# Kernel tuning notes

Hardware: AMD Instinct MI355X
Metric: run time of the kernel (lower is better)

The kernel has to match this reference:

```python
import jax, jax.numpy as jnp
import numpy as np

D_MODEL = 1024
NUM_HEADS = 16
SEQ_LEN = 2048
WINDOW_SIZES = (5, 10, 20, 40)


def _avg_gaussian_mask(seq_len, dtype=jnp.float32):
    # mask[i,j] = exp(-(i-j)^2/(2 w^2)) if j <= i else 0; averaged over 4 windows.
    i = jnp.arange(seq_len, dtype=dtype)[:, None]
    j = jnp.arange(seq_len, dtype=dtype)[None, :]
    d2 = (i - j) ** 2
    lower = (j <= i)
    masks = [jnp.where(lower, jnp.exp(-d2 / (2.0 * w * w)), 0.0) for w in WINDOW_SIZES]
    return sum(masks) / len(WINDOW_SIZES)  # [S, S]


def setup_inputs() -> dict:
    key = jax.random.key(0)
    ks = jax.random.split(key, 11)
    B, S, D = 2, SEQ_LEN, D_MODEL
    std = 1.0 / np.sqrt(D)
    inp = {
        "Q": jax.random.normal(ks[0], (B, S, D), jnp.float32),
        "K": jax.random.normal(ks[1], (B, S, D), jnp.float32),
        "V": jax.random.normal(ks[2], (B, S, D), jnp.float32),
        "Wq": jax.random.uniform(ks[3], (D, D), jnp.float32, -std, std),
        "bq": jax.random.uniform(ks[4], (D,), jnp.float32, -std, std),
        "Wk": jax.random.uniform(ks[5], (D, D), jnp.float32, -std, std),
        "bk": jax.random.uniform(ks[6], (D,), jnp.float32, -std, std),
        "Wv": jax.random.uniform(ks[7], (D, D), jnp.float32, -std, std),
        "bv": jax.random.uniform(ks[8], (D,), jnp.float32, -std, std),
        "Wo": jax.random.uniform(ks[9], (D, D), jnp.float32, -std, std),
        "bo": jax.random.uniform(ks[10], (D,), jnp.float32, -std, std),
    }
    return inp


def reference(Q, K, V, Wq, bq, Wk, bk, Wv, bv, Wo, bo):
    B, S, D = Q.shape
    H, dk = NUM_HEADS, D // NUM_HEADS

    def proj(x, W, b):
        # torch Linear: x @ W^T + b, then split heads -> [B, H, S, dk]
        y = x @ W.T + b
        return y.reshape(B, S, H, dk).transpose(0, 2, 1, 3)

    q = proj(Q, Wq, bq)
    k = proj(K, Wk, bk)
    v = proj(V, Wv, bv)

    # mean over mask dim of (scores + mask_m) == scores + mean(mask)
    avg_mask = _avg_gaussian_mask(S, q.dtype)  # [S, S]
    scores = jnp.einsum('bhqd,bhkd->bhqk', q, k) / jnp.sqrt(jnp.asarray(dk, q.dtype))
    scores = scores + avg_mask  # broadcast over [B, H]
    probs = jax.nn.softmax(scores, axis=-1)
    out = jnp.einsum('bhqk,bhkd->bhqd', probs, v)
    out = out.transpose(0, 2, 1, 3).reshape(B, S, D)
    return out @ Wo.T + bo
```

## Files before the change

### kernel.cpp

```cpp
#include <hip/hip_runtime.h>
#include <hip/hip_bf16.h>


#define S_LEN 2048
#define D_MODEL 1024
#define NHEADS 16
#define DK 64
#define BATCH 2
#define M_ROWS (BATCH * S_LEN)
#define LOG2E 1.4426950408889634f

typedef float f32x4 __attribute__((ext_vector_type(4)));
typedef short s16x8 __attribute__((ext_vector_type(8)));
typedef unsigned short u16x4 __attribute__((ext_vector_type(4)));
typedef unsigned u32x2 __attribute__((ext_vector_type(2)));

__device__ __forceinline__ unsigned short f2bf(float f) {
    unsigned u = __builtin_bit_cast(unsigned, f);
    u = (u + 0x7FFFu + ((u >> 16) & 1u)) >> 16;
    return (unsigned short)u;
}

__device__ __forceinline__ float fast_exp2(float x) {
    float r;
    asm("v_exp_f32 %0, %1" : "=v"(r) : "v"(x));
    return r;
}

__device__ __forceinline__ unsigned cvt_pk_bf16(float a, float b) {
    unsigned r;
    asm("v_cvt_pk_bf16_f32 %0, %1, %2" : "=v"(r) : "v"(a), "v"(b));
    return r;
}

__device__ __forceinline__ float max3f(float a, float b, float c) {
    float r;
    asm("v_max3_f32 %0, %1, %2, %3" : "=v"(r) : "v"(a), "v"(b), "v"(c));
    return r;
}

#define GLD16(gptr, lptr)                                                     \
    __builtin_amdgcn_global_load_lds(                                         \
        (const __attribute__((address_space(1))) void*)(gptr),                \
        (__attribute__((address_space(3))) void*)(lptr), 16, 0, 0)

__global__ __launch_bounds__(256) void convert_kernel(
    const float* __restrict__ Q, const float* __restrict__ K,
    const float* __restrict__ V,
    const float* __restrict__ Wq, const float* __restrict__ Wk,
    const float* __restrict__ Wv, const float* __restrict__ Wo,
    unsigned short* __restrict__ Qb, unsigned short* __restrict__ Kb,
    unsigned short* __restrict__ Vb,
    unsigned short* __restrict__ Wqb, unsigned short* __restrict__ Wkb,
    unsigned short* __restrict__ Wvb, unsigned short* __restrict__ Wob,
    float* __restrict__ mtab)
{
    const int XN = M_ROWS * D_MODEL / 8;
    const int WN = D_MODEL * D_MODEL / 8;
    const int TOT = 3 * XN + 4 * WN;
    int i = blockIdx.x * 256 + threadIdx.x;
    if (i >= TOT) {
        int d = i - TOT;
        if (d < S_LEN) {
            float d2 = (float)d * (float)d;
            mtab[d] = LOG2E * 0.25f * (__expf(-d2 * (1.0f / 50.0f)) +
                                       __expf(-d2 * (1.0f / 200.0f)) +
                                       __expf(-d2 * (1.0f / 800.0f)) +
                                       __expf(-d2 * (1.0f / 3200.0f)));
        }
        return;
    }
    const float* src;
    unsigned short* dst;
    int off;
    if (i < 3 * XN) {
        if (i < XN)          { src = Q; dst = Qb; off = i; }
        else if (i < 2 * XN) { src = K; dst = Kb; off = i - XN; }
        else                 { src = V; dst = Vb; off = i - 2 * XN; }
    } else {
        int j = i - 3 * XN;
        if (j < WN)          { src = Wq; dst = Wqb; off = j; }
        else if (j < 2 * WN) { src = Wk; dst = Wkb; off = j - WN; }
        else if (j < 3 * WN) { src = Wv; dst = Wvb; off = j - 2 * WN; }
        else                 { src = Wo; dst = Wob; off = j - 3 * WN; }
    }
    f32x4 v0 = *(const f32x4*)(src + (size_t)off * 8);
    f32x4 v1 = *(const f32x4*)(src + (size_t)off * 8 + 4);
    s16x8 o;
#pragma unroll
    for (int j = 0; j < 4; ++j) {
        o[j]     = (short)f2bf(v0[j]);
        o[j + 4] = (short)f2bf(v1[j]);
    }
    *(s16x8*)(dst + (size_t)off * 8) = o;
}

__device__ __forceinline__ void gemm_core_128(
    const unsigned short* __restrict__ A, const unsigned short* __restrict__ B,
    unsigned short* As, unsigned short* Bs,
    int m0, int n0, int K, int tid, f32x4 acc[4][4])
{
    const int wid  = tid >> 6;
    const int lane = tid & 63;
    const int g    = lane >> 4;
    const int c    = lane & 15;
    const int wm   = wid >> 1;
    const int wn   = wid & 1;

    const int srow   = tid >> 3;
    const int schunk = tid & 7;

    for (int kt = 0; kt < K / 64; ++kt) {
        const int k0 = kt * 64;
        __syncthreads();
#pragma unroll
        for (int r = 0; r < 4; ++r) {
            const int row = r * 32 + srow;
            GLD16(A + (size_t)(m0 + row) * K + k0 + schunk * 8,
                  &As[(r * 256 + wid * 64) * 8]);
        }
#pragma unroll
        for (int r = 0; r < 4; ++r) {
            const int row = r * 32 + srow;
            GLD16(B + (size_t)(n0 + row) * K + k0 + schunk * 8,
                  &Bs[(r * 256 + wid * 64) * 8]);
        }
        __syncthreads();

        s16x8 a[2][4];
#pragma unroll
        for (int ks = 0; ks < 2; ++ks)
#pragma unroll
            for (int mf = 0; mf < 4; ++mf)
                a[ks][mf] = *(const s16x8*)
                    &As[(wm * 64 + mf * 16 + c) * 64 + ks * 32 + g * 8];
#pragma unroll
        for (int ks = 0; ks < 2; ++ks) {
#pragma unroll
            for (int nf = 0; nf < 4; ++nf) {
                s16x8 b = *(const s16x8*)
                    &Bs[(wn * 64 + nf * 16 + c) * 64 + ks * 32 + g * 8];
#pragma unroll
                for (int mf = 0; mf < 4; ++mf)
                    acc[mf][nf] = __builtin_amdgcn_mfma_f32_16x16x32_bf16(
                        a[ks][mf], b, acc[mf][nf], 0, 0, 0);
            }
        }
    }
}

__global__ __launch_bounds__(256) void proj_gemm(
    const unsigned short* __restrict__ Qx, const unsigned short* __restrict__ Kx,
    const unsigned short* __restrict__ Vx,
    const unsigned short* __restrict__ Wq, const unsigned short* __restrict__ Wk,
    const unsigned short* __restrict__ Wv,
    const float* __restrict__ bq, const float* __restrict__ bk,
    const float* __restrict__ bv,
    unsigned short* __restrict__ qo, unsigned short* __restrict__ ko,
    unsigned short* __restrict__ vo)
{
    const int z = blockIdx.z;
    const unsigned short* X = (z == 0) ? Qx : (z == 1) ? Kx : Vx;
    const unsigned short* W = (z == 0) ? Wq : (z == 1) ? Wk : Wv;
    const float* bias       = (z == 0) ? bq : (z == 1) ? bk : bv;
    unsigned short* out     = (z == 0) ? qo : (z == 1) ? ko : vo;
    const float scale = (z == 0) ? (0.125f * LOG2E) : 1.0f;

    __shared__ unsigned short As[128 * 64];
    __shared__ unsigned short Bs[128 * 64];

    const int tid = threadIdx.x;
    const int flat = blockIdx.y * 32 + blockIdx.x;
    const int sw   = (flat & 7) * 32 + (flat >> 3);
    const int m0   = (sw & 31) * 128;
    const int n0   = (sw >> 5) * 128;

    f32x4 acc[4][4];
#pragma unroll
    for (int i = 0; i < 4; ++i)
#pragma unroll
        for (int j = 0; j < 4; ++j) acc[i][j] = (f32x4){0.f, 0.f, 0.f, 0.f};

    gemm_core_128(X, W, As, Bs, m0, n0, D_MODEL, tid, acc);

    const int lane = tid & 63;
    const int g    = lane >> 4;
    const int c    = lane & 15;
    const int wm   = (tid >> 6) >> 1;
    const int wn   = (tid >> 6) & 1;

#pragma unroll
    for (int mf = 0; mf < 4; ++mf) {
#pragma unroll
        for (int nf = 0; nf < 4; ++nf) {
            const int o = n0 + wn * 64 + nf * 16 + c;
            const float bv_ = bias[o];
            const int h  = o >> 6;
            const int dd = o & 63;
#pragma unroll
            for (int r = 0; r < 4; ++r) {
                const int m = m0 + wm * 64 + mf * 16 + g * 4 + r;
                const int b = m >> 11;
                const int s = m & (S_LEN - 1);
                const float val = (acc[mf][nf][r] + bv_) * scale;
                out[(((size_t)(b * NHEADS + h)) * S_LEN + s) * DK + dd] = f2bf(val);
            }
        }
    }
}

__global__ __launch_bounds__(256) void out_gemm(
    const unsigned short* __restrict__ A,
    const unsigned short* __restrict__ W,
    const float* __restrict__ bias,
    float* __restrict__ out)
{
    __shared__ unsigned short As[128 * 64];
    __shared__ unsigned short Bs[128 * 64];

    const int tid = threadIdx.x;
    const int flat = blockIdx.y * 32 + blockIdx.x;
    const int sw   = (flat & 7) * 32 + (flat >> 3);
    const int m0   = (sw & 31) * 128;
    const int n0   = (sw >> 5) * 128;

    f32x4 acc[4][4];
#pragma unroll
    for (int i = 0; i < 4; ++i)
#pragma unroll
        for (int j = 0; j < 4; ++j) acc[i][j] = (f32x4){0.f, 0.f, 0.f, 0.f};

    gemm_core_128(A, W, As, Bs, m0, n0, D_MODEL, tid, acc);

    const int lane = tid & 63;
    const int g    = lane >> 4;
    const int c    = lane & 15;
    const int wm   = (tid >> 6) >> 1;
    const int wn   = (tid >> 6) & 1;

#pragma unroll
    for (int mf = 0; mf < 4; ++mf) {
#pragma unroll
        for (int nf = 0; nf < 4; ++nf) {
            const int o = n0 + wn * 64 + nf * 16 + c;
            const float bv_ = bias[o];
#pragma unroll
            for (int r = 0; r < 4; ++r) {
                const int m = m0 + wm * 64 + mf * 16 + g * 4 + r;
                out[(size_t)m * D_MODEL + o] = acc[mf][nf][r] + bv_;
            }
        }
    }
}

#define VSWZ(row) ((((row) >> 1) & 7) << 4)

__global__ __launch_bounds__(512) void attn_kernel(
    const unsigned short* __restrict__ qh,
    const unsigned short* __restrict__ kh,
    const unsigned short* __restrict__ vh,
    const float* __restrict__ mask_tab,
    unsigned short* __restrict__ attn_out)
{
    __shared__ float mtab[S_LEN];
    __shared__ unsigned short Kt[64 * 64];
    __shared__ unsigned short Vt[64 * 64];
    __shared__ unsigned short Pt[8][16 * 64];

    const int tid  = threadIdx.x;
    const int wid  = tid >> 6;
    const int lane = tid & 63;
    const int g    = lane >> 4;
    const int c    = lane & 15;

    const int flat = blockIdx.y * 16 + blockIdx.x;
    const int sw   = (flat & 7) * 64 + (flat >> 3);
    const int bh   = sw >> 4;
    const int bx   = sw & 15;
    const int b    = bh >> 4;
    const int h    = bh & 15;
    const int q0w  = bx * 128 + wid * 16;

    *(f32x4*)&mtab[tid * 4] = *(const f32x4*)&mask_tab[tid * 4];

    const size_t head_off = (size_t)bh * S_LEN * DK;
    const unsigned short* qp = qh + head_off;
    const unsigned short* kp = kh + head_off;
    const unsigned short* vp = vh + head_off;

    s16x8 aq[2];
    {
        const unsigned short* qrow = qp + (size_t)(q0w + c) * DK;
        aq[0] = *(const s16x8*)(qrow + g * 8);
        aq[1] = *(const s16x8*)(qrow + 32 + g * 8);
    }

    f32x4 acc_o[4];
#pragma unroll
    for (int nf = 0; nf < 4; ++nf) acc_o[nf] = (f32x4){0.f, 0.f, 0.f, 0.f};
    float m_l = -1e30f;
    f32x4 lsum = (f32x4){0.f, 0.f, 0.f, 0.f};

    const int srowK = tid >> 3;
    const int soffE = (tid & 7) * 8;
    const int vd0   = (tid & 31) * 2;
    const int vkq   = (tid >> 5) * 4;

    s16x8 kreg;
    unsigned vreg[4];
    kreg = *(const s16x8*)&kp[(size_t)srowK * DK + soffE];
#pragma unroll
    for (int i = 0; i < 4; ++i)
        vreg[i] = *(const unsigned*)&vp[(size_t)(vkq + i) * DK + vd0];

    unsigned short* Ptw = Pt[wid];

    for (int kt = 0; kt < S_LEN / 64; ++kt) {
        const int k0 = kt * 64;
        __syncthreads();

        *(s16x8*)((char*)Kt + srowK * 128 + ((soffE * 2) ^ ((srowK & 7) << 4))) = kreg;
        {
            u16x4 lo4, hi4;
#pragma unroll
            for (int i = 0; i < 4; ++i) {
                lo4[i] = (unsigned short)vreg[i];
                hi4[i] = (unsigned short)(vreg[i] >> 16);
            }
            *(u16x4*)((char*)Vt + vd0 * 128 + ((vkq * 2) ^ VSWZ(vd0))) = lo4;
            *(u16x4*)((char*)Vt + (vd0 + 1) * 128 +
                      ((vkq * 2) ^ VSWZ(vd0 + 1))) = hi4;
        }
        if (kt < S_LEN / 64 - 1) {
            const int k1 = k0 + 64;
            kreg = *(const s16x8*)&kp[(size_t)(k1 + srowK) * DK + soffE];
#pragma unroll
            for (int i = 0; i < 4; ++i)
                vreg[i] = *(const unsigned*)&vp[(size_t)(k1 + vkq + i) * DK + vd0];
        }
        __syncthreads();

        f32x4 st[4];
        __builtin_amdgcn_s_setprio(1);
#pragma unroll
        for (int nf = 0; nf < 4; ++nf) {
            st[nf] = (f32x4){0.f, 0.f, 0.f, 0.f};
#pragma unroll
            for (int f = 0; f < 2; ++f) {
                const int row = nf * 16 + c;
                s16x8 kf = *(const s16x8*)((const char*)Kt + row * 128 +
                                           ((f * 64 + g * 16) ^ ((row & 7) << 4)));
                st[nf] = __builtin_amdgcn_mfma_f32_16x16x32_bf16(
                    kf, aq[f], st[nf], 0, 0, 0);
            }
        }
        __builtin_amdgcn_s_setprio(0);

        const int diff = q0w - k0;
        if (diff >= -15 && diff <= 510) {
            const int dbase = q0w + c - k0;
#pragma unroll
            for (int nf = 0; nf < 4; ++nf) {
#pragma unroll
                for (int r = 0; r < 4; ++r) {
                    const int d = dbase - (nf * 16 + g * 4 + r);
                    if (d >= 0) st[nf][r] += mtab[d];
                }
            }
        }

        float tm = max3f(st[0][0], st[0][1], st[0][2]);
        tm = max3f(tm, st[0][3], st[1][0]);
        tm = max3f(tm, st[1][1], st[1][2]);
        tm = max3f(tm, st[1][3], st[2][0]);
        tm = max3f(tm, st[2][1], st[2][2]);
        tm = max3f(tm, st[2][3], st[3][0]);
        tm = max3f(tm, st[3][1], st[3][2]);
        tm = fmaxf(tm, st[3][3]);

        if (__any(tm > m_l + 8.0f)) {
            tm = fmaxf(tm, __shfl_xor(tm, 16));
            tm = fmaxf(tm, __shfl_xor(tm, 32));
            const float mnew = fmaxf(m_l, tm);
            const float csc  = fast_exp2(m_l - mnew);
            m_l = mnew;
            lsum *= csc;
            f32x4 cscv;
#pragma unroll
            for (int r = 0; r < 4; ++r) cscv[r] = __shfl(csc, g * 4 + r);
#pragma unroll
            for (int nf = 0; nf < 4; ++nf) acc_o[nf] *= cscv;
        }

#pragma unroll
        for (int nf = 0; nf < 4; ++nf)
#pragma unroll
            for (int r = 0; r < 4; ++r)
                st[nf][r] = fast_exp2(st[nf][r] - m_l);
        lsum += (st[0] + st[1]) + (st[2] + st[3]);

#pragma unroll
        for (int nf = 0; nf < 4; ++nf) {
            u32x2 pk;
            pk[0] = cvt_pk_bf16(st[nf][0], st[nf][1]);
            pk[1] = cvt_pk_bf16(st[nf][2], st[nf][3]);
            *(u32x2*)((char*)Ptw + c * 128 +
                      ((nf * 32 + g * 8) ^ ((c & 7) << 4))) = pk;
        }

        __builtin_amdgcn_s_setprio(1);
#pragma unroll
        for (int f = 0; f < 2; ++f) {
            s16x8 pa = *(const s16x8*)((const char*)Ptw + c * 128 +
                                       ((f * 64 + g * 16) ^ ((c & 7) << 4)));
#pragma unroll
            for (int nf = 0; nf < 4; ++nf) {
                const int row = nf * 16 + c;
                s16x8 vb = *(const s16x8*)((const char*)Vt + row * 128 +
                                           ((f * 64 + g * 16) ^ VSWZ(row)));
                acc_o[nf] = __builtin_amdgcn_mfma_f32_16x16x32_bf16(
                    pa, vb, acc_o[nf], 0, 0, 0);
            }
        }
        __builtin_amdgcn_s_setprio(0);
    }

    float l = (lsum[0] + lsum[1]) + (lsum[2] + lsum[3]);
    l += __shfl_xor(l, 16);
    l += __shfl_xor(l, 32);
    f32x4 linv;
#pragma unroll
    for (int r = 0; r < 4; ++r) linv[r] = 1.0f / __shfl(l, g * 4 + r);
#pragma unroll
    for (int nf = 0; nf < 4; ++nf) {
#pragma unroll
        for (int r = 0; r < 4; ++r) {
            const int i_glob = q0w + g * 4 + r;
            const int d = nf * 16 + c;
            attn_out[((size_t)(b * S_LEN + i_glob)) * D_MODEL + h * DK + d] =
                f2bf(acc_o[nf][r] * linv[r]);
        }
    }
}

extern "C" void kernel_launch(void* const* d_in, const int* in_sizes, int n_in,
                              void* d_out, int out_size, void* d_ws, size_t ws_size,
                              hipStream_t stream) {
    const float* Q  = (const float*)d_in[0];
    const float* K  = (const float*)d_in[1];
    const float* V  = (const float*)d_in[2];
    const float* Wq = (const float*)d_in[3];
    const float* bq = (const float*)d_in[4];
    const float* Wk = (const float*)d_in[5];
    const float* bk = (const float*)d_in[6];
    const float* Wv = (const float*)d_in[7];
    const float* bv = (const float*)d_in[8];
    const float* Wo = (const float*)d_in[9];
    const float* bo = (const float*)d_in[10];
    float* out = (float*)d_out;

    const size_t XE = (size_t)M_ROWS * D_MODEL;
    const size_t WE = (size_t)D_MODEL * D_MODEL;
    unsigned short* qh  = (unsigned short*)d_ws;
    unsigned short* kh  = qh + XE;
    unsigned short* vh  = kh + XE;
    unsigned short* ah  = vh + XE;
    unsigned short* Qb  = ah + XE;
    unsigned short* Kb  = Qb + XE;
    unsigned short* Vb  = Kb + XE;
    unsigned short* Wqb = Vb + XE;
    unsigned short* Wkb = Wqb + WE;
    unsigned short* Wvb = Wkb + WE;
    unsigned short* Wob = Wvb + WE;
    float* mtab = (float*)(Wob + WE);

    convert_kernel<<<dim3((3 * XE / 8 + 4 * WE / 8) / 256 + 8), 256, 0, stream>>>(
        Q, K, V, Wq, Wk, Wv, Wo, Qb, Kb, Vb, Wqb, Wkb, Wvb, Wob, mtab);
    proj_gemm<<<dim3(32, 8, 3), 256, 0, stream>>>(
        Qb, Kb, Vb, Wqb, Wkb, Wvb, bq, bk, bv, qh, kh, vh);
    attn_kernel<<<dim3(16, 32), 512, 0, stream>>>(
        qh, kh, vh, mtab, ah);
    out_gemm<<<dim3(32, 8), 256, 0, stream>>>(
        ah, Wob, bo, out);
}
```

Baseline: 135.4 us.

## Switch attention to 32x32x16 MFMA with register-resident P via permlane32 swap

The attention kernel moves from 16x16x32 to 32x32x16 bf16 MFMAs. Each wave now handles 32 query rows, so the block shrinks to 4 waves of 256 threads. The softmax probabilities are packed to bf16 and rearranged across half-waves with v_permlane32_swap, so they feed the PV MFMA straight from registers instead of round-tripping through a per-wave LDS buffer. This drops the P shared-memory traffic and cuts MFMA instruction count per tile. In exchange it raises register pressure and halves the waves per block, which may reduce latency hiding.

```diff
diff --git a/kernel.cpp b/kernel.cpp
--- a/kernel.cpp
+++ b/kernel.cpp
@@ -11,9 +11,10 @@
 #define LOG2E 1.4426950408889634f
 
 typedef float f32x4 __attribute__((ext_vector_type(4)));
+typedef float f32x16 __attribute__((ext_vector_type(16)));
 typedef short s16x8 __attribute__((ext_vector_type(8)));
-typedef unsigned short u16x4 __attribute__((ext_vector_type(4)));
-typedef unsigned u32x2 __attribute__((ext_vector_type(2)));
+typedef unsigned short u16x8 __attribute__((ext_vector_type(8)));
+typedef unsigned u32x4 __attribute__((ext_vector_type(4)));
 
 __device__ __forceinline__ unsigned short f2bf(float f) {
     unsigned u = __builtin_bit_cast(unsigned, f);
@@ -253,9 +254,10 @@
     }
 }
 
+#define KSWZ(row) (((row) & 7) << 4)
 #define VSWZ(row) ((((row) >> 1) & 7) << 4)
 
-__global__ __launch_bounds__(512) void attn_kernel(
+__global__ __launch_bounds__(256) void attn_kernel(
     const unsigned short* __restrict__ qh,
     const unsigned short* __restrict__ kh,
     const unsigned short* __restrict__ vh,
@@ -265,13 +267,12 @@
     __shared__ float mtab[S_LEN];
     __shared__ unsigned short Kt[64 * 64];
     __shared__ unsigned short Vt[64 * 64];
-    __shared__ unsigned short Pt[8][16 * 64];
 
     const int tid  = threadIdx.x;
     const int wid  = tid >> 6;
     const int lane = tid & 63;
-    const int g    = lane >> 4;
-    const int c    = lane & 15;
+    const int l31  = lane & 31;
+    const int hi   = lane >> 5;
 
     const int flat = blockIdx.y * 16 + blockIdx.x;
     const int sw   = (flat & 7) * 64 + (flat >> 3);
@@ -279,167 +280,163 @@
     const int bx   = sw & 15;
     const int b    = bh >> 4;
     const int h    = bh & 15;
-    const int q0w  = bx * 128 + wid * 16;
-
-    *(f32x4*)&mtab[tid * 4] = *(const f32x4*)&mask_tab[tid * 4];
+    const int q0w  = bx * 128 + wid * 32;
+
+    *(f32x4*)&mtab[tid * 8]     = *(const f32x4*)&mask_tab[tid * 8];
+    *(f32x4*)&mtab[tid * 8 + 4] = *(const f32x4*)&mask_tab[tid * 8 + 4];
 
     const size_t head_off = (size_t)bh * S_LEN * DK;
     const unsigned short* qp = qh + head_off;
     const unsigned short* kp = kh + head_off;
     const unsigned short* vp = vh + head_off;
 
-    s16x8 aq[2];
+    s16x8 qf[4];
     {
-        const unsigned short* qrow = qp + (size_t)(q0w + c) * DK;
-        aq[0] = *(const s16x8*)(qrow + g * 8);
-        aq[1] = *(const s16x8*)(qrow + 32 + g * 8);
-    }
-
-    f32x4 acc_o[4];
-#pragma unroll
-    for (int nf = 0; nf < 4; ++nf) acc_o[nf] = (f32x4){0.f, 0.f, 0.f, 0.f};
+        const unsigned short* qrow = qp + (size_t)(q0w + l31) * DK;
+#pragma unroll
+        for (int ks = 0; ks < 4; ++ks)
+            qf[ks] = *(const s16x8*)(qrow + ks * 16 + hi * 8);
+    }
+
+    f32x16 acc[2];
+    acc[0] = {};
+    acc[1] = {};
     float m_l = -1e30f;
     f32x4 lsum = (f32x4){0.f, 0.f, 0.f, 0.f};
 
-    const int srowK = tid >> 3;
-    const int soffE = (tid & 7) * 8;
-    const int vd0   = (tid & 31) * 2;
-    const int vkq   = (tid >> 5) * 4;
-
-    s16x8 kreg;
-    unsigned vreg[4];
-    kreg = *(const s16x8*)&kp[(size_t)srowK * DK + soffE];
-#pragma unroll
-    for (int i = 0; i < 4; ++i)
-        vreg[i] = *(const unsigned*)&vp[(size_t)(vkq + i) * DK + vd0];
-
-    unsigned short* Ptw = Pt[wid];
+    const int krow = tid >> 2;
+    const int kcol = (tid & 3) * 16;
+    const int vd0  = (tid & 31) * 2;
+    const int vk8  = (tid >> 5) * 8;
+
+    s16x8 kr0, kr1;
+    unsigned vr[8];
+    kr0 = *(const s16x8*)&kp[(size_t)krow * DK + kcol];
+    kr1 = *(const s16x8*)&kp[(size_t)krow * DK + kcol + 8];
+#pragma unroll
+    for (int i = 0; i < 8; ++i)
+        vr[i] = *(const unsigned*)&vp[(size_t)(vk8 + i) * DK + vd0];
 
     for (int kt = 0; kt < S_LEN / 64; ++kt) {
         const int k0 = kt * 64;
         __syncthreads();
 
-        *(s16x8*)((char*)Kt + srowK * 128 + ((soffE * 2) ^ ((srowK & 7) << 4))) = kreg;
         {
-            u16x4 lo4, hi4;
-#pragma unroll
-            for (int i = 0; i < 4; ++i) {
-                lo4[i] = (unsigned short)vreg[i];
-                hi4[i] = (unsigned short)(vreg[i] >> 16);
+            char* kb = (char*)Kt + krow * 128;
+            *(s16x8*)(kb + ((kcol * 2) ^ KSWZ(krow)))      = kr0;
+            *(s16x8*)(kb + ((kcol * 2 + 16) ^ KSWZ(krow))) = kr1;
+            u16x8 lo, hi8;
+#pragma unroll
+            for (int i = 0; i < 8; ++i) {
+                lo[i]  = (unsigned short)vr[i];
+                hi8[i] = (unsigned short)(vr[i] >> 16);
             }
-            *(u16x4*)((char*)Vt + vd0 * 128 + ((vkq * 2) ^ VSWZ(vd0))) = lo4;
-            *(u16x4*)((char*)Vt + (vd0 + 1) * 128 +
-                      ((vkq * 2) ^ VSWZ(vd0 + 1))) = hi4;
+            *(u16x8*)((char*)Vt + vd0 * 128 + ((vk8 * 2) ^ VSWZ(vd0)))           = lo;
+            *(u16x8*)((char*)Vt + (vd0 + 1) * 128 + ((vk8 * 2) ^ VSWZ(vd0 + 1))) = hi8;
         }
         if (kt < S_LEN / 64 - 1) {
             const int k1 = k0 + 64;
-            kreg = *(const s16x8*)&kp[(size_t)(k1 + srowK) * DK + soffE];
-#pragma unroll
-            for (int i = 0; i < 4; ++i)
-                vreg[i] = *(const unsigned*)&vp[(size_t)(k1 + vkq + i) * DK + vd0];
+            kr0 = *(const s16x8*)&kp[(size_t)(k1 + krow) * DK + kcol];
+            kr1 = *(const s16x8*)&kp[(size_t)(k1 + krow) * DK + kcol + 8];
+#pragma unroll
+            for (int i = 0; i < 8; ++i)
+                vr[i] = *(const unsigned*)&vp[(size_t)(k1 + vk8 + i) * DK + vd0];
         }
         __syncthreads();
 
-        f32x4 st[4];
+        f32x16 st[2];
+        st[0] = {};
+        st[1] = {};
         __builtin_amdgcn_s_setprio(1);
 #pragma unroll
-        for (int nf = 0; nf < 4; ++nf) {
-            st[nf] = (f32x4){0.f, 0.f, 0.f, 0.f};
-#pragma unroll
-            for (int f = 0; f < 2; ++f) {
-                const int row = nf * 16 + c;
-                s16x8 kf = *(const s16x8*)((const char*)Kt + row * 128 +
-                                           ((f * 64 + g * 16) ^ ((row & 7) << 4)));
-                st[nf] = __builtin_amdgcn_mfma_f32_16x16x32_bf16(
-                    kf, aq[f], st[nf], 0, 0, 0);
-            }
+        for (int ks = 0; ks < 4; ++ks) {
+            const int off = ks * 32 + hi * 16;
+            s16x8 kf0 = *(const s16x8*)((const char*)Kt + l31 * 128 +
+                                        (off ^ KSWZ(l31)));
+            s16x8 kf1 = *(const s16x8*)((const char*)Kt + (32 + l31) * 128 +
+                                        (off ^ KSWZ(l31)));
+            st[0] = __builtin_amdgcn_mfma_f32_32x32x16_bf16(kf0, qf[ks], st[0], 0, 0, 0);
+            st[1] = __builtin_amdgcn_mfma_f32_32x32x16_bf16(kf1, qf[ks], st[1], 0, 0, 0);
         }
         __builtin_amdgcn_s_setprio(0);
 
         const int diff = q0w - k0;
-        if (diff >= -15 && diff <= 510) {
-            const int dbase = q0w + c - k0;
-#pragma unroll
-            for (int nf = 0; nf < 4; ++nf) {
-#pragma unroll
-                for (int r = 0; r < 4; ++r) {
-                    const int d = dbase - (nf * 16 + g * 4 + r);
-                    if (d >= 0) st[nf][r] += mtab[d];
+        if (diff >= -31 && diff <= 510) {
+            const int dq = q0w + l31 - k0 - 4 * hi;
+#pragma unroll
+            for (int t = 0; t < 2; ++t)
+#pragma unroll
+                for (int r = 0; r < 16; ++r) {
+                    const int d = dq - (t * 32 + (r & 3) + 8 * (r >> 2));
+                    if (d >= 0) st[t][r] += mtab[d];
                 }
-            }
-        }
-
-        float tm = max3f(st[0][0], st[0][1], st[0][2]);
-        tm = max3f(tm, st[0][3], st[1][0]);
-        tm = max3f(tm, st[1][1], st[1][2]);
-        tm = max3f(tm, st[1][3], st[2][0]);
-        tm = max3f(tm, st[2][1], st[2][2]);
-        tm = max3f(tm, st[2][3], st[3][0]);
-        tm = max3f(tm, st[3][1], st[3][2]);
-        tm = fmaxf(tm, st[3][3]);
+        }
+
+        float tm = fmaxf(st[0][0], st[0][1]);
+#pragma unroll
+        for (int r = 2; r < 16; r += 2) tm = max3f(tm, st[0][r], st[0][r + 1]);
+#pragma unroll
+        for (int r = 0; r < 16; r += 2) tm = max3f(tm, st[1][r], st[1][r + 1]);
+        tm = fmaxf(tm, __shfl_xor(tm, 32));
 
         if (__any(tm > m_l + 8.0f)) {
-            tm = fmaxf(tm, __shfl_xor(tm, 16));
-            tm = fmaxf(tm, __shfl_xor(tm, 32));
             const float mnew = fmaxf(m_l, tm);
             const float csc  = fast_exp2(m_l - mnew);
             m_l = mnew;
             lsum *= csc;
-            f32x4 cscv;
-#pragma unroll
-            for (int r = 0; r < 4; ++r) cscv[r] = __shfl(csc, g * 4 + r);
-#pragma unroll
-            for (int nf = 0; nf < 4; ++nf) acc_o[nf] *= cscv;
-        }
-
-#pragma unroll
-        for (int nf = 0; nf < 4; ++nf)
-#pragma unroll
-            for (int r = 0; r < 4; ++r)
-                st[nf][r] = fast_exp2(st[nf][r] - m_l);
-        lsum += (st[0] + st[1]) + (st[2] + st[3]);
-
-#pragma unroll
-        for (int nf = 0; nf < 4; ++nf) {
-            u32x2 pk;
-            pk[0] = cvt_pk_bf16(st[nf][0], st[nf][1]);
-            pk[1] = cvt_pk_bf16(st[nf][2], st[nf][3]);
-            *(u32x2*)((char*)Ptw + c * 128 +
-                      ((nf * 32 + g * 8) ^ ((c & 7) << 4))) = pk;
-        }
+#pragma unroll
+            for (int r = 0; r < 16; ++r) {
+                const int q_r = (r & 3) + 8 * (r >> 2) + 4 * hi;
+                const float cr = __shfl(csc, q_r);
+                acc[0][r] *= cr;
+                acc[1][r] *= cr;
+            }
+        }
+
+#pragma unroll
+        for (int t = 0; t < 2; ++t)
+#pragma unroll
+            for (int r = 0; r < 16; ++r)
+                st[t][r] = fast_exp2(st[t][r] - m_l);
+#pragma unroll
+        for (int t = 0; t < 2; ++t)
+#pragma unroll
+            for (int r = 0; r < 16; ++r) lsum[r & 3] += st[t][r];
 
         __builtin_amdgcn_s_setprio(1);
 #pragma unroll
-        for (int f = 0; f < 2; ++f) {
-            s16x8 pa = *(const s16x8*)((const char*)Ptw + c * 128 +
-                                       ((f * 64 + g * 16) ^ ((c & 7) << 4)));
-#pragma unroll
-            for (int nf = 0; nf < 4; ++nf) {
-                const int row = nf * 16 + c;
-                s16x8 vb = *(const s16x8*)((const char*)Vt + row * 128 +
-                                           ((f * 64 + g * 16) ^ VSWZ(row)));
-                acc_o[nf] = __builtin_amdgcn_mfma_f32_16x16x32_bf16(
-                    pa, vb, acc_o[nf], 0, 0, 0);
-            }
+        for (int s = 0; s < 4; ++s) {
+            const int t  = s >> 1;
+            const int b8 = (s & 1) * 8;
+            unsigned w0 = cvt_pk_bf16(st[t][b8 + 0], st[t][b8 + 1]);
+            unsigned w1 = cvt_pk_bf16(st[t][b8 + 2], st[t][b8 + 3]);
+            unsigned w2 = cvt_pk_bf16(st[t][b8 + 4], st[t][b8 + 5]);
+            unsigned w3 = cvt_pk_bf16(st[t][b8 + 6], st[t][b8 + 7]);
+            asm("v_permlane32_swap_b32 %0, %1" : "+v"(w0), "+v"(w2));
+            asm("v_permlane32_swap_b32 %0, %1" : "+v"(w1), "+v"(w3));
+            u32x4 u = (u32x4){w0, w1, w2, w3};
+            s16x8 pa = __builtin_bit_cast(s16x8, u);
+            const int off = s * 32 + hi * 16;
+            s16x8 vb0 = *(const s16x8*)((const char*)Vt + l31 * 128 +
+                                        (off ^ VSWZ(l31)));
+            s16x8 vb1 = *(const s16x8*)((const char*)Vt + (32 + l31) * 128 +
+                                        (off ^ VSWZ(32 + l31)));
+            acc[0] = __builtin_amdgcn_mfma_f32_32x32x16_bf16(pa, vb0, acc[0], 0, 0, 0);
+            acc[1] = __builtin_amdgcn_mfma_f32_32x32x16_bf16(pa, vb1, acc[1], 0, 0, 0);
         }
         __builtin_amdgcn_s_setprio(0);
     }
 
     float l = (lsum[0] + lsum[1]) + (lsum[2] + lsum[3]);
-    l += __shfl_xor(l, 16);
     l += __shfl_xor(l, 32);
-    f32x4 linv;
-#pragma unroll
-    for (int r = 0; r < 4; ++r) linv[r] = 1.0f / __shfl(l, g * 4 + r);
-#pragma unroll
-    for (int nf = 0; nf < 4; ++nf) {
-#pragma unroll
-        for (int r = 0; r < 4; ++r) {
-            const int i_glob = q0w + g * 4 + r;
-            const int d = nf * 16 + c;
-            attn_out[((size_t)(b * S_LEN + i_glob)) * D_MODEL + h * DK + d] =
-                f2bf(acc_o[nf][r] * linv[r]);
-        }
+    const float linv = 1.0f / l;
+#pragma unroll
+    for (int r = 0; r < 16; ++r) {
+        const int q_r = (r & 3) + 8 * (r >> 2) + 4 * hi;
+        const float lr = __shfl(linv, q_r);
+        const size_t row = (size_t)(b * S_LEN + q0w + q_r) * D_MODEL + h * DK;
+        attn_out[row + l31]      = f2bf(acc[0][r] * lr);
+        attn_out[row + 32 + l31] = f2bf(acc[1][r] * lr);
     }
 }
 
@@ -478,7 +475,7 @@
         Q, K, V, Wq, Wk, Wv, Wo, Qb, Kb, Vb, Wqb, Wkb, Wvb, Wob, mtab);
     proj_gemm<<<dim3(32, 8, 3), 256, 0, stream>>>(
         Qb, Kb, Vb, Wqb, Wkb, Wvb, bq, bk, bv, qh, kh, vh);
-    attn_kernel<<<dim3(16, 32), 512, 0, stream>>>(
+    attn_kernel<<<dim3(16, 32), 256, 0, stream>>>(
         qh, kh, vh, mtab, ah);
     out_gemm<<<dim3(32, 8), 256, 0, stream>>>(
         ah, Wob, bo, out);
```

After: 146.8 us. 8.4% more time.

## Double-buffer K/V tiles in attention kernel to halve block barriers

Applied to the files above, without the earlier changes.

K and V shared-memory tiles are now double-buffered. Each iteration writes the next tile into the alternate buffer while computing on the current one, so only one __syncthreads per iteration is needed instead of two. This is meant to cut barrier stalls and let the LDS stores overlap with the MFMA work. In exchange it uses 16KB more LDS per block, which could lower occupancy.

```diff
diff --git a/kernel.cpp b/kernel.cpp
--- a/kernel.cpp
+++ b/kernel.cpp
@@ -253,6 +253,7 @@
     }
 }
 
+#define KSWZ(row) (((row) & 7) << 4)
 #define VSWZ(row) ((((row) >> 1) & 7) << 4)
 
 __global__ __launch_bounds__(512) void attn_kernel(
@@ -263,8 +264,8 @@
     unsigned short* __restrict__ attn_out)
 {
     __shared__ float mtab[S_LEN];
-    __shared__ unsigned short Kt[64 * 64];
-    __shared__ unsigned short Vt[64 * 64];
+    __shared__ unsigned short Kt[2][64 * 64];
+    __shared__ unsigned short Vt[2][64 * 64];
     __shared__ unsigned short Pt[8][16 * 64];
 
     const int tid  = threadIdx.x;
@@ -306,39 +307,59 @@
     const int vd0   = (tid & 31) * 2;
     const int vkq   = (tid >> 5) * 4;
 
+    unsigned short* Ptw = Pt[wid];
+
     s16x8 kreg;
     unsigned vreg[4];
+
     kreg = *(const s16x8*)&kp[(size_t)srowK * DK + soffE];
 #pragma unroll
     for (int i = 0; i < 4; ++i)
         vreg[i] = *(const unsigned*)&vp[(size_t)(vkq + i) * DK + vd0];
-
-    unsigned short* Ptw = Pt[wid];
-
-    for (int kt = 0; kt < S_LEN / 64; ++kt) {
+    {
+        *(s16x8*)((char*)Kt[0] + srowK * 128 + ((soffE * 2) ^ KSWZ(srowK))) = kreg;
+        u16x4 lo4, hi4;
+#pragma unroll
+        for (int i = 0; i < 4; ++i) {
+            lo4[i] = (unsigned short)vreg[i];
+            hi4[i] = (unsigned short)(vreg[i] >> 16);
+        }
+        *(u16x4*)((char*)Vt[0] + vd0 * 128 + ((vkq * 2) ^ VSWZ(vd0)))           = lo4;
+        *(u16x4*)((char*)Vt[0] + (vd0 + 1) * 128 + ((vkq * 2) ^ VSWZ(vd0 + 1))) = hi4;
+    }
+    kreg = *(const s16x8*)&kp[(size_t)(64 + srowK) * DK + soffE];
+#pragma unroll
+    for (int i = 0; i < 4; ++i)
+        vreg[i] = *(const unsigned*)&vp[(size_t)(64 + vkq + i) * DK + vd0];
+    __syncthreads();
+
+    const int NT = S_LEN / 64;
+    for (int kt = 0; kt < NT; ++kt) {
         const int k0 = kt * 64;
-        __syncthreads();
-
-        *(s16x8*)((char*)Kt + srowK * 128 + ((soffE * 2) ^ ((srowK & 7) << 4))) = kreg;
-        {
+        const int cur = kt & 1;
+        const unsigned short* Kc = Kt[cur];
+        const unsigned short* Vc = Vt[cur];
+
+        if (kt + 1 < NT) {
+            unsigned short* Kn = Kt[cur ^ 1];
+            unsigned short* Vn = Vt[cur ^ 1];
+            *(s16x8*)((char*)Kn + srowK * 128 + ((soffE * 2) ^ KSWZ(srowK))) = kreg;
             u16x4 lo4, hi4;
 #pragma unroll
             for (int i = 0; i < 4; ++i) {
                 lo4[i] = (unsigned short)vreg[i];
                 hi4[i] = (unsigned short)(vreg[i] >> 16);
             }
-            *(u16x4*)((char*)Vt + vd0 * 128 + ((vkq * 2) ^ VSWZ(vd0))) = lo4;
-            *(u16x4*)((char*)Vt + (vd0 + 1) * 128 +
-                      ((vkq * 2) ^ VSWZ(vd0 + 1))) = hi4;
-        }
-        if (kt < S_LEN / 64 - 1) {
-            const int k1 = k0 + 64;
-            kreg = *(const s16x8*)&kp[(size_t)(k1 + srowK) * DK + soffE];
-#pragma unroll
-            for (int i = 0; i < 4; ++i)
-                vreg[i] = *(const unsigned*)&vp[(size_t)(k1 + vkq + i) * DK + vd0];
-        }
-        __syncthreads();
+            *(u16x4*)((char*)Vn + vd0 * 128 + ((vkq * 2) ^ VSWZ(vd0)))           = lo4;
+            *(u16x4*)((char*)Vn + (vd0 + 1) * 128 + ((vkq * 2) ^ VSWZ(vd0 + 1))) = hi4;
+            if (kt + 2 < NT) {
+                const int k2 = k0 + 128;
+                kreg = *(const s16x8*)&kp[(size_t)(k2 + srowK) * DK + soffE];
+#pragma unroll
+                for (int i = 0; i < 4; ++i)
+                    vreg[i] = *(const unsigned*)&vp[(size_t)(k2 + vkq + i) * DK + vd0];
+            }
+        }
 
         f32x4 st[4];
         __builtin_amdgcn_s_setprio(1);
@@ -348,8 +369,8 @@
 #pragma unroll
             for (int f = 0; f < 2; ++f) {
                 const int row = nf * 16 + c;
-                s16x8 kf = *(const s16x8*)((const char*)Kt + row * 128 +
-                                           ((f * 64 + g * 16) ^ ((row & 7) << 4)));
+                s16x8 kf = *(const s16x8*)((const char*)Kc + row * 128 +
+                                           ((f * 64 + g * 16) ^ KSWZ(row)));
                 st[nf] = __builtin_amdgcn_mfma_f32_16x16x32_bf16(
                     kf, aq[f], st[nf], 0, 0, 0);
             }
@@ -405,24 +426,26 @@
             pk[0] = cvt_pk_bf16(st[nf][0], st[nf][1]);
             pk[1] = cvt_pk_bf16(st[nf][2], st[nf][3]);
             *(u32x2*)((char*)Ptw + c * 128 +
-                      ((nf * 32 + g * 8) ^ ((c & 7) << 4))) = pk;
+                      ((nf * 32 + g * 8) ^ KSWZ(c))) = pk;
         }
 
         __builtin_amdgcn_s_setprio(1);
 #pragma unroll
         for (int f = 0; f < 2; ++f) {
             s16x8 pa = *(const s16x8*)((const char*)Ptw + c * 128 +
-                                       ((f * 64 + g * 16) ^ ((c & 7) << 4)));
+                                       ((f * 64 + g * 16) ^ KSWZ(c)));
 #pragma unroll
             for (int nf = 0; nf < 4; ++nf) {
                 const int row = nf * 16 + c;
-                s16x8 vb = *(const s16x8*)((const char*)Vt + row * 128 +
+                s16x8 vb = *(const s16x8*)((const char*)Vc + row * 128 +
                                            ((f * 64 + g * 16) ^ VSWZ(row)));
                 acc_o[nf] = __builtin_amdgcn_mfma_f32_16x16x32_bf16(
                     pa, vb, acc_o[nf], 0, 0, 0);
             }
         }
         __builtin_amdgcn_s_setprio(0);
+
+        __syncthreads();
     }
 
     float l = (lsum[0] + lsum[1]) + (lsum[2] + lsum[3]);
```

New measurement: 135.6 us. Within noise of the previous version (+0.2%).
